# Kernel tuning notes

Measured on AMD Instinct MI355X. Metric: run time of the kernel, lower is better.

Reference implementation:

```python
import jax, jax.numpy as jnp
import numpy as np

B, S_SRC, T, D, H, DFF, NC, L = 8, 256, 64, 256, 8, 1024, 128, 2
HD = D // H
EPS = 1e-5


def _pe(length, d):
    pos = jnp.arange(length, dtype=jnp.float32)[:, None]
    div = jnp.exp(jnp.arange(0, d, 2, dtype=jnp.float32) * (-np.log(10000.0) / d))
    pe = jnp.zeros((length, d), dtype=jnp.float32)
    pe = pe.at[:, 0::2].set(jnp.sin(pos * div))
    pe = pe.at[:, 1::2].set(jnp.cos(pos * div))
    return pe


def setup_inputs() -> dict:
    key = jax.random.key(0)
    ks = jax.random.split(key, 16)
    s = 0.02
    rn = lambda k, shape: jax.random.normal(k, shape, dtype=jnp.float32) * s
    return {
        "encoder_output": jax.random.normal(ks[0], (B, S_SRC, D), dtype=jnp.float32),
        "emb_w": rn(ks[1], (D, NC)), "emb_b": jnp.zeros((D,), jnp.float32),
        "sa_wqkv": rn(ks[2], (L, 3 * D, D)), "sa_bqkv": jnp.zeros((L, 3 * D), jnp.float32),
        "sa_wo": rn(ks[3], (L, D, D)), "sa_bo": jnp.zeros((L, D), jnp.float32),
        "ca_wqkv": rn(ks[4], (L, 3 * D, D)), "ca_bqkv": jnp.zeros((L, 3 * D), jnp.float32),
        "ca_wo": rn(ks[5], (L, D, D)), "ca_bo": jnp.zeros((L, D), jnp.float32),
        "ln1_g": jnp.ones((L, D), jnp.float32), "ln1_b": jnp.zeros((L, D), jnp.float32),
        "ln2_g": jnp.ones((L, D), jnp.float32), "ln2_b": jnp.zeros((L, D), jnp.float32),
        "ffn_w1": rn(ks[6], (L, DFF, D)), "ffn_b1": jnp.zeros((L, DFF), jnp.float32),
        "ffn_w2": rn(ks[7], (L, D, DFF)), "ffn_b2": jnp.zeros((L, D), jnp.float32),
        "ln3_g": jnp.ones((L, D), jnp.float32), "ln3_b": jnp.zeros((L, D), jnp.float32),
        "op_w1": rn(ks[8], (D, D)), "op_b1": jnp.zeros((D,), jnp.float32),
        "bn_g": jnp.ones((D,), jnp.float32), "bn_b": jnp.zeros((D,), jnp.float32),
        "op_w2": rn(ks[9], (NC, D)), "op_b2": jnp.zeros((NC,), jnp.float32),
        "tgt_length": T,
    }


def _ln(x, g, b):
    m = x.mean(-1, keepdims=True)
    v = ((x - m) ** 2).mean(-1, keepdims=True)
    return (x - m) * jax.lax.rsqrt(v + EPS) * g + b


def _heads(x):  # [B,T,D] -> [B,H,T,HD]
    b, t, _ = x.shape
    return x.reshape(b, t, H, HD).transpose(0, 2, 1, 3)


def _merge(x):  # [B,H,T,HD] -> [B,T,D]
    return x.transpose(0, 2, 1, 3).reshape(x.shape[0], -1, D)


def _forward(encoder_output, emb_w, emb_b, sa_wqkv, sa_bqkv, sa_wo, sa_bo,
             ca_wqkv, ca_bqkv, ca_wo, ca_bo, ln1_g, ln1_b, ln2_g, ln2_b,
             ffn_w1, ffn_b1, ffn_w2, ffn_b2, ln3_g, ln3_b,
             op_w1, op_b1, bn_g, bn_b, op_w2, op_b2, tgt_length):
    Tq = tgt_length
    pe = _pe(Tq, D)
    scale = 1.0 / np.sqrt(HD)
    causal = jnp.where(jnp.arange(Tq)[:, None] >= jnp.arange(Tq)[None, :], 0.0, -1e9).astype(jnp.float32)
    # cross-attention K/V from encoder memory (constant across decode steps)
    mem_kv = jnp.einsum('bsd,led->lbse', encoder_output, ca_wqkv[:, D:, :]) + ca_bqkv[:, None, None, D:]
    mem_k = mem_kv[..., :D].reshape(L, B, S_SRC, H, HD).transpose(0, 1, 3, 2, 4)
    mem_v = mem_kv[..., D:].reshape(L, B, S_SRC, H, HD).transpose(0, 1, 3, 2, 4)

    def decode_full(buf):  # buf [B,Tq,NC] -> logits [B,Tq,NC]
        x = buf @ emb_w.T + emb_b + pe[None]
        for l in range(L):
            qkv = x @ sa_wqkv[l].T + sa_bqkv[l]
            q, k, v = (_heads(qkv[..., i * D:(i + 1) * D]) for i in range(3))
            att = jax.nn.softmax(jnp.einsum('bhqe,bhke->bhqk', q, k) * scale + causal, axis=-1)
            o = _merge(jnp.einsum('bhqk,bhke->bhqe', att, v)) @ sa_wo[l].T + sa_bo[l]
            x = _ln(x + o, ln1_g[l], ln1_b[l])
            qc = _heads(x @ ca_wqkv[l, :D].T + ca_bqkv[l, :D])
            attc = jax.nn.softmax(jnp.einsum('bhqe,bhke->bhqk', qc, mem_k[l]) * scale, axis=-1)
            oc = _merge(jnp.einsum('bhqk,bhke->bhqe', attc, mem_v[l])) @ ca_wo[l].T + ca_bo[l]
            x = _ln(x + oc, ln2_g[l], ln2_b[l])
            f = jax.nn.relu(x @ ffn_w1[l].T + ffn_b1[l]) @ ffn_w2[l].T + ffn_b2[l]
            x = _ln(x + f, ln3_g[l], ln3_b[l])
        y = x @ op_w1.T + op_b1
        # eval-mode BatchNorm1d with running stats (0, 1): pure affine
        y = jax.nn.relu(y * (1.0 / np.sqrt(1.0 + EPS)) * bn_g + bn_b)
        return y @ op_w2.T + op_b2

    def step(buf, t):
        out = decode_full(buf)                                   # [B,Tq,NC]
        y_t = jax.lax.dynamic_slice_in_dim(out, t, 1, axis=1)    # [B,1,NC]
        buf = jax.lax.dynamic_update_slice_in_dim(buf, y_t, jnp.minimum(t + 1, Tq - 1), axis=1)
        return buf, y_t[:, 0]

    buf0 = jnp.zeros((B, Tq, NC), dtype=jnp.float32)  # decoder_input starts as zeros
    _, ys = jax.lax.scan(step, buf0, jnp.arange(Tq))
    return ys.transpose(1, 0, 2)  # [B,Tq,NC]


def reference(encoder_output, emb_w, emb_b, sa_wqkv, sa_bqkv, sa_wo, sa_bo,
              ca_wqkv, ca_bqkv, ca_wo, ca_bo, ln1_g, ln1_b, ln2_g, ln2_b,
              ffn_w1, ffn_b1, ffn_w2, ffn_b2, ln3_g, ln3_b,
              op_w1, op_b1, bn_g, bn_b, op_w2, op_b2, tgt_length):
    return _forward(encoder_output, emb_w, emb_b, sa_wqkv, sa_bqkv, sa_wo, sa_bo,
                    ca_wqkv, ca_bqkv, ca_wo, ca_bo, ln1_g, ln1_b, ln2_g, ln2_b,
                    ffn_w1, ffn_b1, ffn_w2, ffn_b2, ln3_g, ln3_b,
                    op_w1, op_b1, bn_g, bn_b, op_w2, op_b2, tgt_length)
```

## Files before the change

### kernel.cpp

```cpp
#include <hip/hip_runtime.h>
#include <math.h>


#define EPS_ 1e-5f
#define SCALE_ 0.17677669529663687f
#define BNS 0.99999500003749969f
#define DEV __device__ __forceinline__
#define DYNF 36864

#define D4(a,b) ((a).x*(b).x+(a).y*(b).y+(a).z*(b).z+(a).w*(b).w)
#define F4(p)  (*(float4*)(p))
#define CF4(p) (*(const float4*)(p))

DEV float ald(const float* p){return __hip_atomic_load(p,__ATOMIC_RELAXED,__HIP_MEMORY_SCOPE_AGENT);}
DEV void  ast(float* p,float v){__hip_atomic_store(p,v,__ATOMIC_RELAXED,__HIP_MEMORY_SCOPE_AGENT);}
DEV int   aldi(const int* p){return __hip_atomic_load(p,__ATOMIC_RELAXED,__HIP_MEMORY_SCOPE_AGENT);}
DEV void  asti(int* p,int v){__hip_atomic_store(p,v,__ATOMIC_RELAXED,__HIP_MEMORY_SCOPE_AGENT);}

DEV float wsum(float v){
#pragma unroll
  for(int o=32;o;o>>=1) v+=__shfl_xor(v,o,64);
  return v;
}
DEV float wmax(float v){
#pragma unroll
  for(int o=32;o;o>>=1) v=fmaxf(v,__shfl_xor(v,o,64));
  return v;
}

DEV void waitflags(const int* base,int n,int s){
  if((int)threadIdx.x<64){
    const int* p=base+threadIdx.x*32;
    bool need=(int)threadIdx.x<n;
    int v=need?aldi(p):0x7fffffff;
    while(!__all(v>=s)){ v=need?aldi(p):0x7fffffff; }
  }
  __syncthreads();
}

template<int NB>
DEV void ln_reg(float (&v)[NB],const float* __restrict__ g,
                const float* __restrict__ bb,float* red){
  int tid=threadIdx.x,wid=tid>>6,lane=tid&63;
  float s[NB],s2[NB];
#pragma unroll
  for(int r=0;r<NB;++r){ s[r]=wsum(v[r]); s2[r]=wsum(v[r]*v[r]); }
  if(lane==0){
#pragma unroll
    for(int r=0;r<NB;++r){ red[r*4+wid]=s[r]; red[NB*4+r*4+wid]=s2[r]; }
  }
  __syncthreads();
  float gv=g[tid],bv=bb[tid];
#pragma unroll
  for(int r=0;r<NB;++r){
    float S=red[r*4+0]+red[r*4+1]+red[r*4+2]+red[r*4+3];
    float S2=red[NB*4+r*4+0]+red[NB*4+r*4+1]+red[NB*4+r*4+2]+red[NB*4+r*4+3];
    float m=S*(1.f/256.f);
    float rs=rsqrtf(S2*(1.f/256.f)-m*m+EPS_);
    v[r]=(v[r]-m)*rs*gv+bv;
  }
}

template<int NB,int L>
DEV void role_s1(float* LDS,int h,int bs,
    const float* __restrict__ sa_wqkv,const float* __restrict__ sa_bqkv,
    const float* __restrict__ sa_wo,
    const float* __restrict__ ln2_g,const float* __restrict__ ln2_b,
    const float* __restrict__ ln3_g,const float* __restrict__ ln3_b,
    const float* __restrict__ ffn_b2,const float* __restrict__ emb_b,
    int* F1,const int* F3,const int* FX0,const int* FER2,int* FER3,
    float* kc,float* vc,const float* r2red,float* r3red,
    const float* p3,float* p1,const float* xrow){
  const int tid=threadIdx.x;
  float* W   =LDS;
  float* WO  =LDS+24960;
  float* XS  =LDS+34176;
  float* QKV =LDS+35200;
  float* SC  =LDS+35584;
  float* PART=LDS+35840;
  float* RED =LDS+36096;

  for(int idx=tid;idx<96*64;idx+=256){
    int row=idx>>6,i4=idx&63,which=row>>5,j=row&31;
    F4(&W[row*260+4*i4])=CF4(sa_wqkv+(size_t)L*196608+((size_t)(which*256+h*32+j))*256+4*i4);
  }
  for(int idx=tid;idx<256*8;idx+=256){
    int c=idx>>3,i=idx&7;
    F4(&WO[c*36+4*i])=CF4(sa_wo+(size_t)L*65536+(size_t)c*256+h*32+4*i);
  }
  __syncthreads();

  float dv=expf((float)(tid&~1)*(-9.210340371976184f/256.f));

  for(int t=0;t<64;++t){
    if(L==0){
      float aarg=(float)t*dv;
      float peb=emb_b[tid]+((tid&1)?cosf(aarg):sinf(aarg));
      waitflags(FX0+bs*32,NB,t);
#pragma unroll
      for(int bi=0;bi<NB;++bi) XS[bi*256+tid]=ald(xrow+(bs+bi)*256+tid)+peb;
      __syncthreads();
    }else{
      waitflags(FER2+bs*32,NB,t+1);
      float r2v[NB];
#pragma unroll
      for(int bi=0;bi<NB;++bi) r2v[bi]=ald(r2red+(bs+bi)*256+tid);
      ln_reg<NB>(r2v,ln2_g,ln2_b,RED);
      waitflags(F3+bs*16*32,NB*16,t+1);
      float p3v[NB][16];
#pragma unroll
      for(int bi=0;bi<NB;++bi)
#pragma unroll
        for(int cg=0;cg<16;++cg) p3v[bi][cg]=ald(p3+(cg*8+bs+bi)*256+tid);
      float r3v[NB];
      float fb=ffn_b2[tid];
#pragma unroll
      for(int bi=0;bi<NB;++bi){
        float s=0.f;
#pragma unroll
        for(int cg=0;cg<16;++cg) s+=p3v[bi][cg];
        r3v[bi]=r2v[bi]+s+fb;
      }
      if(h==0){
#pragma unroll
        for(int bi=0;bi<NB;++bi) ast(r3red+(bs+bi)*256+tid,r3v[bi]);
        __syncthreads();
        if(tid<NB) asti(FER3+(bs+tid)*32,t+1);
      }
      ln_reg<NB>(r3v,ln3_g,ln3_b,RED+32);
#pragma unroll
      for(int bi=0;bi<NB;++bi) XS[bi*256+tid]=r3v[bi];
      __syncthreads();
    }
    if(tid<192){
      int row=tid>>1,kq=tid&1;
      float a[NB];
#pragma unroll
      for(int bi=0;bi<NB;++bi) a[bi]=0.f;
#pragma unroll
      for(int i=0;i<32;++i){
        float4 w=F4(&W[row*260+kq*128+4*i]);
#pragma unroll
        for(int bi=0;bi<NB;++bi) a[bi]+=D4(w,F4(&XS[bi*256+kq*128+4*i]));
      }
#pragma unroll
      for(int bi=0;bi<NB;++bi) a[bi]+=__shfl_down(a[bi],1,64);
      if(kq==0){
        int which=row>>5,j=row&31;
        float bias=sa_bqkv[L*768+which*256+h*32+j];
#pragma unroll
        for(int bi=0;bi<NB;++bi){
          float v=a[bi]+bias;
          if(which==0) QKV[bi*96+j]=v;
          else{
            int off=(which==1)?32:64;
            QKV[bi*96+off+j]=v;
            float* cache=(which==1)?kc:vc;
            cache[(((size_t)L*64+(bs+bi)*8+h)*64+t)*32+j]=v;
          }
        }
      }
    }
    __syncthreads();
    {
      int bi=(tid>>6)&(NB-1),key=tid&63;
      float s=-3.0e38f;
      if(key<=t){
        float a=0.f;
        if(key==t){
#pragma unroll
          for(int i=0;i<8;++i) a+=D4(F4(&QKV[bi*96+4*i]),F4(&QKV[bi*96+32+4*i]));
        }else{
          const float4* kr=(const float4*)(kc+(((size_t)L*64+(bs+bi)*8+h)*64+key)*32);
#pragma unroll
          for(int i=0;i<8;++i) a+=D4(F4(&QKV[bi*96+4*i]),kr[i]);
        }
        s=a*SCALE_;
      }
      float mx=wmax(s);
      float e=(key<=t)?expf(s-mx):0.f;
      float sm=wsum(e);
      SC[bi*64+key]=e/sm;
    }
    __syncthreads();
    {
      int bi=(tid>>6)&(NB-1),lane=tid&63,gg=lane>>5,col=lane&31;
      float acc=0.f;
      int k0=gg*32,k1=min(k0+32,t+1);
      for(int k=k0;k<k1;++k){
        float vv=(k==t)?QKV[bi*96+64+col]
                       :vc[(((size_t)L*64+(bs+bi)*8+h)*64+k)*32+col];
        acc+=SC[bi*64+k]*vv;
      }
      PART[bi*64+gg*32+col]=acc;
    }
    __syncthreads();
    if(tid<NB*32){
      int bi=tid>>5,col=tid&31;
      QKV[bi*96+col]=PART[bi*64+col]+PART[bi*64+32+col];
    }
    __syncthreads();
    {
      float a[NB];
#pragma unroll
      for(int bi=0;bi<NB;++bi) a[bi]=0.f;
#pragma unroll
      for(int i=0;i<8;++i){
        float4 w=F4(&WO[tid*36+4*i]);
#pragma unroll
        for(int bi=0;bi<NB;++bi) a[bi]+=D4(w,F4(&QKV[bi*96+4*i]));
      }
#pragma unroll
      for(int bi=0;bi<NB;++bi) ast(p1+(h*8+bs+bi)*256+tid,a[bi]);
    }
    __syncthreads();
    if(tid<NB) asti(F1+((L*8+bs+tid)*8+h)*32,t+1);
  }
}

DEV void role_s2(float* LDS,int rid,
    const float* __restrict__ enc,
    const float* __restrict__ ca_wqkv,const float* __restrict__ ca_bqkv,
    const float* __restrict__ ca_wo,
    const float* __restrict__ ln1_g,const float* __restrict__ ln1_b,
    const float* __restrict__ ln3_g,const float* __restrict__ ln3_b,
    const float* __restrict__ sa_bo,const float* __restrict__ emb_b,
    const int* F1,int* F2,const int* FX0,const int* FER3,int* FER1,
    const float* r3red,float* r1red,const float* p1,float* p2,const float* xrow){
  const int tid=threadIdx.x;
  const int b=rid>>4,h=(rid>>1)&7,l=rid&1;
  float* WQ  =LDS;
  float* WO  =LDS+8320;
  float* MK  =LDS+17536;
  float* MV  =LDS+26752;
  float* XS  =LDS+35968;
  float* PS  =LDS+36224;
  float* PART=LDS+36480;
  float* QC  =LDS+36736;
  float* RED =LDS+36784;

  for(int idx=tid;idx<64*64;idx+=256){
    int row=idx>>6,i4=idx&63;
    int grow=(row<32)?(256+h*32+row):(512+h*32+row-32);
    F4(&LDS[row*260+4*i4])=CF4(ca_wqkv+(size_t)l*196608+(size_t)grow*256+4*i4);
  }
  __syncthreads();
  for(int p=0;p<2;++p){
    int s=p*128+(tid>>1),kh=tid&1;
    float4 er[32];
#pragma unroll
    for(int i=0;i<32;++i) er[i]=CF4(enc+((size_t)(b*256+s))*256+kh*128+4*i);
    for(int out=0;out<64;++out){
      float a=0.f;
#pragma unroll
      for(int i=0;i<32;++i) a+=D4(F4(&LDS[out*260+kh*128+4*i]),er[i]);
      a+=__shfl_down(a,1,64);
      if(kh==0){
        if(out<32) MK[s*36+out]    =a+ca_bqkv[l*768+256+h*32+out];
        else       MV[s*36+out-32] =a+ca_bqkv[l*768+512+h*32+out-32];
      }
    }
  }
  __syncthreads();
  for(int idx=tid;idx<32*64;idx+=256){
    int row=idx>>6,i4=idx&63;
    F4(&WQ[row*260+4*i4])=CF4(ca_wqkv+(size_t)l*196608+(size_t)(h*32+row)*256+4*i4);
  }
  for(int idx=tid;idx<256*8;idx+=256){
    int c=idx>>3,i=idx&7;
    F4(&WO[c*36+4*i])=CF4(ca_wo+(size_t)l*65536+(size_t)c*256+h*32+4*i);
  }
  __syncthreads();

  float dv=expf((float)(tid&~1)*(-9.210340371976184f/256.f));

  for(int t=0;t<64;++t){
    float xv;
    if(l==0){
      float aarg=(float)t*dv;
      float peb=emb_b[tid]+((tid&1)?cosf(aarg):sinf(aarg));
      waitflags(FX0+b*32,1,t);
      xv=ald(xrow+b*256+tid)+peb;
    }else{
      waitflags(FER3+b*32,1,t+1);
      float t0[1]={ald(r3red+b*256+tid)};
      ln_reg<1>(t0,ln3_g,ln3_b,RED);
      xv=t0[0];
    }
    waitflags(F1+(l*8+b)*8*32,8,t+1);
    float p1v[8];
#pragma unroll
    for(int h2=0;h2<8;++h2) p1v[h2]=ald(p1+(h2*8+b)*256+tid);
    float r1v=xv+sa_bo[l*256+tid];
#pragma unroll
    for(int h2=0;h2<8;++h2) r1v+=p1v[h2];
    if(h==0){
      ast(r1red+l*2048+b*256+tid,r1v);
      __syncthreads();
      if(tid==0) asti(FER1+(l*8+b)*32,t+1);
    }
    float t1[1]={r1v};
    ln_reg<1>(t1,ln1_g+l*256,ln1_b+l*256,RED+8);
    XS[tid]=t1[0];
    __syncthreads();
    {
      int col=tid>>3,g=tid&7;
      float a=0.f;
#pragma unroll
      for(int i=0;i<8;++i) a+=D4(F4(&WQ[col*260+g*32+4*i]),F4(&XS[g*32+4*i]));
      a+=__shfl_down(a,4,64);a+=__shfl_down(a,2,64);a+=__shfl_down(a,1,64);
      if(g==0) QC[col]=a+ca_bqkv[l*768+h*32+col];
    }
    __syncthreads();
    {
      float a=0.f;
#pragma unroll
      for(int i=0;i<8;++i) a+=D4(F4(&MK[tid*36+4*i]),F4(&QC[4*i]));
      float sv=a*SCALE_;
      int wid=tid>>6,lane=tid&63;
      float mw=wmax(sv);
      float e=expf(sv-mw);
      float sw=wsum(e);
      if(lane==0){RED[16+wid]=mw;RED[20+wid]=sw;}
      __syncthreads();
      float M=fmaxf(fmaxf(RED[16],RED[17]),fmaxf(RED[18],RED[19]));
      float tot=RED[20]*expf(RED[16]-M)+RED[21]*expf(RED[17]-M)
               +RED[22]*expf(RED[18]-M)+RED[23]*expf(RED[19]-M);
      PS[tid]=e*expf(mw-M)/tot;
    }
    __syncthreads();
    {
      int gg=tid>>5,col=tid&31;
      float acc=0.f;
      for(int s2=gg*32;s2<gg*32+32;++s2) acc+=PS[s2]*MV[s2*36+col];
      PART[gg*32+col]=acc;
    }
    __syncthreads();
    if(tid<32){
      float o=0.f;
#pragma unroll
      for(int g2=0;g2<8;++g2) o+=PART[g2*32+tid];
      QC[tid]=o;
    }
    __syncthreads();
    {
      float a=0.f;
#pragma unroll
      for(int i=0;i<8;++i) a+=D4(F4(&WO[tid*36+4*i]),F4(&QC[4*i]));
      ast(p2+(h*8+b)*256+tid,a);
    }
    __syncthreads();
    if(tid==0) asti(F2+((l*8+b)*8+h)*32,t+1);
  }
}

DEV void role_s3(float* LDS,int rid,
    const float* __restrict__ ffn_w1,const float* __restrict__ ffn_b1,
    const float* __restrict__ ffn_w2,
    const float* __restrict__ ln1_g,const float* __restrict__ ln1_b,
    const float* __restrict__ ln2_g,const float* __restrict__ ln2_b,
    const float* __restrict__ ca_bo,
    const int* F2,int* F3,const int* FER1,int* FER2,
    const float* r1red,float* r2red,const float* p2,float* p3){
  const int tid=threadIdx.x;
  const int l=rid>>5,cg=(rid>>1)&15,bh=rid&1,bs=bh*4;
  float* W1 =LDS;
  float* W2T=LDS+16640;
  float* X4 =LDS+33280;
  float* HH =LDS+34304;
  float* RED=LDS+34576;

  for(int idx=tid;idx<64*64;idx+=256){
    int row=idx>>6,i4=idx&63;
    F4(&W1[row*260+4*i4])=CF4(ffn_w1+(size_t)l*262144+(size_t)(cg*64+row)*256+4*i4);
  }
  for(int idx=tid;idx<256*16;idx+=256){
    int cc=idx>>4,k4=idx&15;
    float4 w=CF4(ffn_w2+(size_t)l*262144+(size_t)cc*1024+cg*64+4*k4);
    W2T[(4*k4+0)*260+cc]=w.x;W2T[(4*k4+1)*260+cc]=w.y;
    W2T[(4*k4+2)*260+cc]=w.z;W2T[(4*k4+3)*260+cc]=w.w;
  }
  __syncthreads();

  for(int t=0;t<64;++t){
    waitflags(FER1+(l*8+bs)*32,4,t+1);
    float r1v[4];
#pragma unroll
    for(int bi=0;bi<4;++bi) r1v[bi]=ald(r1red+l*2048+(bs+bi)*256+tid);
    ln_reg<4>(r1v,ln1_g+l*256,ln1_b+l*256,RED);
    waitflags(F2+(l*8+bs)*8*32,32,t+1);
    float p2v[4][8];
#pragma unroll
    for(int bi=0;bi<4;++bi)
#pragma unroll
      for(int h2=0;h2<8;++h2) p2v[bi][h2]=ald(p2+(h2*8+bs+bi)*256+tid);
    float r2v[4];
    float cb=ca_bo[l*256+tid];
#pragma unroll
    for(int bi=0;bi<4;++bi){
      float s=0.f;
#pragma unroll
      for(int h2=0;h2<8;++h2) s+=p2v[bi][h2];
      r2v[bi]=r1v[bi]+s+cb;
    }
    if(cg==0){
#pragma unroll
      for(int bi=0;bi<4;++bi) ast(r2red+l*2048+(bs+bi)*256+tid,r2v[bi]);
      __syncthreads();
      if(tid<4) asti(FER2+(l*8+bs+tid)*32,t+1);
    }
    ln_reg<4>(r2v,ln2_g+l*256,ln2_b+l*256,RED+32);
#pragma unroll
    for(int bi=0;bi<4;++bi) X4[bi*256+tid]=r2v[bi];
    __syncthreads();
    {
      int row=tid>>2,kq=tid&3;
      float a0=0.f,a1=0.f,a2=0.f,a3=0.f;
#pragma unroll
      for(int i=0;i<16;++i){
        float4 w=F4(&W1[row*260+kq*64+4*i]);
        a0+=D4(w,F4(&X4[0*256+kq*64+4*i]));a1+=D4(w,F4(&X4[1*256+kq*64+4*i]));
        a2+=D4(w,F4(&X4[2*256+kq*64+4*i]));a3+=D4(w,F4(&X4[3*256+kq*64+4*i]));
      }
      a0+=__shfl_down(a0,2,64);a0+=__shfl_down(a0,1,64);
      a1+=__shfl_down(a1,2,64);a1+=__shfl_down(a1,1,64);
      a2+=__shfl_down(a2,2,64);a2+=__shfl_down(a2,1,64);
      a3+=__shfl_down(a3,2,64);a3+=__shfl_down(a3,1,64);
      if(kq==0){
        float b1v=ffn_b1[l*1024+cg*64+row];
        HH[0*68+row]=fmaxf(a0+b1v,0.f);HH[1*68+row]=fmaxf(a1+b1v,0.f);
        HH[2*68+row]=fmaxf(a2+b1v,0.f);HH[3*68+row]=fmaxf(a3+b1v,0.f);
      }
    }
    __syncthreads();
    {
      int chunk=tid&63,bi=tid>>6;
      float ax=0.f,ay=0.f,az=0.f,aw=0.f;
      for(int k=0;k<64;++k){
        float4 w=F4(&W2T[k*260+4*chunk]);
        float hv=HH[bi*68+k];
        ax+=w.x*hv;ay+=w.y*hv;az+=w.z*hv;aw+=w.w*hv;
      }
      float* dst=p3+(size_t)l*32768+(size_t)(cg*8+bs+bi)*256+4*chunk;
      ast(dst+0,ax);ast(dst+1,ay);ast(dst+2,az);ast(dst+3,aw);
    }
    __syncthreads();
    if(tid<4) asti(F3+((l*8+bs+tid)*16+cg)*32,t+1);
  }
}

DEV void role_head(float* LDS,int b,
    const float* __restrict__ op_w1,const float* __restrict__ op_b1,
    const float* __restrict__ bn_g,const float* __restrict__ bn_b,
    const float* __restrict__ op_w2,const float* __restrict__ op_b2,
    const float* __restrict__ emb_w,
    const float* __restrict__ ln2_g,const float* __restrict__ ln2_b,
    const float* __restrict__ ln3_g,const float* __restrict__ ln3_b,
    const float* __restrict__ ffn_b2,
    const int* F3,int* FX0,const int* FER2,
    const float* r2red,const float* p3,float* xrow,float* outp){
  const int tid=threadIdx.x;
  float* X  =LDS;
  float* Y  =LDS+256;
  float* LG =LDS+512;
  float* RED=LDS+768;

  for(int t=0;t<64;++t){
    waitflags(FER2+(8+b)*32,1,t+1);
    float t0[1]={ald(r2red+2048+b*256+tid)};
    ln_reg<1>(t0,ln2_g+256,ln2_b+256,RED);
    waitflags(F3+(8+b)*16*32,16,t+1);
    float p3v[16];
#pragma unroll
    for(int cg=0;cg<16;++cg) p3v[cg]=ald(p3+32768+(cg*8+b)*256+tid);
    float r3=t0[0]+ffn_b2[256+tid];
#pragma unroll
    for(int cg=0;cg<16;++cg) r3+=p3v[cg];
    float t1[1]={r3};
    ln_reg<1>(t1,ln3_g+256,ln3_b+256,RED+8);
    X[tid]=t1[0];
    __syncthreads();
    {
      int g=tid&15,cc=tid>>4;
      for(int it=0;it<16;++it){
        int c2=it*16+cc;
        const float4* w4=(const float4*)(op_w1+(size_t)c2*256+g*16);
        const float4* x4=(const float4*)(X+g*16);
        float a=0.f;
#pragma unroll
        for(int i=0;i<4;++i) a+=D4(w4[i],x4[i]);
        a+=__shfl_down(a,8,64);a+=__shfl_down(a,4,64);
        a+=__shfl_down(a,2,64);a+=__shfl_down(a,1,64);
        if(g==0){
          float y=a+op_b1[c2];
          Y[c2]=fmaxf(y*BNS*bn_g[c2]+bn_b[c2],0.f);
        }
      }
    }
    __syncthreads();
    {
      int g=tid&15,cc=tid>>4;
      for(int it=0;it<8;++it){
        int c2=it*16+cc;
        const float4* w4=(const float4*)(op_w2+(size_t)c2*256+g*16);
        const float4* y4=(const float4*)(Y+g*16);
        float a=0.f;
#pragma unroll
        for(int i=0;i<4;++i) a+=D4(w4[i],y4[i]);
        a+=__shfl_down(a,8,64);a+=__shfl_down(a,4,64);
        a+=__shfl_down(a,2,64);a+=__shfl_down(a,1,64);
        if(g==0){
          float v=a+op_b2[c2];
          LG[c2]=v;
          outp[((size_t)b*64+t)*128+c2]=v;
        }
      }
    }
    __syncthreads();
    if(t<63){
      int g=tid&7,cc=tid>>3;
      for(int it=0;it<8;++it){
        int c2=it*32+cc;
        const float4* w4=(const float4*)(emb_w+(size_t)c2*128+g*16);
        const float4* l4=(const float4*)(LG+g*16);
        float a=0.f;
#pragma unroll
        for(int i=0;i<4;++i) a+=D4(w4[i],l4[i]);
        a+=__shfl_down(a,4,64);a+=__shfl_down(a,2,64);a+=__shfl_down(a,1,64);
        if(g==0) ast(xrow+b*256+c2,a);
      }
    }
    __syncthreads();
    if(tid==0) asti(FX0+b*32,t+1);
  }
}


__global__ void __launch_bounds__(256,1) k_decode(
    const float* enc,const float* emb_w,const float* emb_b,
    const float* sa_wqkv,const float* sa_bqkv,const float* sa_wo,const float* sa_bo,
    const float* ca_wqkv,const float* ca_bqkv,const float* ca_wo,const float* ca_bo,
    const float* ln1_g,const float* ln1_b,const float* ln2_g,const float* ln2_b,
    const float* ffn_w1,const float* ffn_b1,const float* ffn_w2,const float* ffn_b2,
    const float* ln3_g,const float* ln3_b,
    const float* op_w1,const float* op_b1,const float* bn_g,const float* bn_b,
    const float* op_w2,const float* op_b2,
    int* FX0,int* FER1,int* FER2,int* FER3,int* F1,int* F2,int* F3,
    float* xrow,float* kc,float* vc,float* r1red,float* r2red,float* r3red,
    float* p1,float* p2,float* p3,float* outp){
  __shared__ __align__(16) float LDS[DYNF];
  const int blk=blockIdx.x;
  if(blk<16){
    role_s1<4,0>(LDS,blk>>1,(blk&1)*4,sa_wqkv,sa_bqkv,sa_wo,ln2_g,ln2_b,ln3_g,ln3_b,
                 ffn_b2,emb_b,F1,F3,FX0,FER2,FER3,kc,vc,r2red,r3red,p3,p1,xrow);
  }else if(blk<48){
    int r=blk-16;
    role_s1<2,1>(LDS,r>>2,(r&3)*2,sa_wqkv,sa_bqkv,sa_wo,ln2_g,ln2_b,ln3_g,ln3_b,
                 ffn_b2,emb_b,F1,F3,FX0,FER2,FER3,kc,vc,r2red,r3red,p3,p1,xrow);
  }else if(blk<176){
    role_s2(LDS,blk-48,enc,ca_wqkv,ca_bqkv,ca_wo,ln1_g,ln1_b,ln3_g,ln3_b,sa_bo,emb_b,
            F1,F2,FX0,FER3,FER1,r3red,r1red,p1,p2,xrow);
  }else if(blk<240){
    role_s3(LDS,blk-176,ffn_w1,ffn_b1,ffn_w2,ln1_g,ln1_b,ln2_g,ln2_b,ca_bo,
            F2,F3,FER1,FER2,r1red,r2red,p2,p3);
  }else{
    role_head(LDS,blk-240,op_w1,op_b1,bn_g,bn_b,op_w2,op_b2,emb_w,
              ln2_g,ln2_b,ln3_g,ln3_b,ffn_b2,F3,FX0,FER2,r2red,p3,xrow,outp);
  }
}


extern "C" void kernel_launch(void* const* d_in, const int* in_sizes, int n_in,
                              void* d_out, int out_size, void* d_ws, size_t ws_size,
                              hipStream_t stream) {
  (void)in_sizes;(void)n_in;(void)out_size;(void)ws_size;
  const float* enc     =(const float*)d_in[0];
  const float* emb_w   =(const float*)d_in[1];
  const float* emb_b   =(const float*)d_in[2];
  const float* sa_wqkv =(const float*)d_in[3];
  const float* sa_bqkv =(const float*)d_in[4];
  const float* sa_wo   =(const float*)d_in[5];
  const float* sa_bo   =(const float*)d_in[6];
  const float* ca_wqkv =(const float*)d_in[7];
  const float* ca_bqkv =(const float*)d_in[8];
  const float* ca_wo   =(const float*)d_in[9];
  const float* ca_bo   =(const float*)d_in[10];
  const float* ln1_g   =(const float*)d_in[11];
  const float* ln1_b   =(const float*)d_in[12];
  const float* ln2_g   =(const float*)d_in[13];
  const float* ln2_b   =(const float*)d_in[14];
  const float* ffn_w1  =(const float*)d_in[15];
  const float* ffn_b1  =(const float*)d_in[16];
  const float* ffn_w2  =(const float*)d_in[17];
  const float* ffn_b2  =(const float*)d_in[18];
  const float* ln3_g   =(const float*)d_in[19];
  const float* ln3_b   =(const float*)d_in[20];
  const float* op_w1   =(const float*)d_in[21];
  const float* op_b1   =(const float*)d_in[22];
  const float* bn_g    =(const float*)d_in[23];
  const float* bn_b    =(const float*)d_in[24];
  const float* op_w2   =(const float*)d_in[25];
  const float* op_b2   =(const float*)d_in[26];

  float* out=(float*)d_out;

  int* I=(int*)d_ws;
  int* FX0 =I;
  int* FER1=I+256;
  int* FER2=I+768;
  int* FER3=I+1280;
  int* F1  =I+1536;
  int* F2  =I+5632;
  int* F3  =I+9728;
  hipMemsetAsync(d_ws,0,17920*4+2048*4,stream);

  float* F=(float*)d_ws+17920;
  float* xrow =F;
  float* kc   =xrow+2048;
  float* vc   =kc+262144;
  float* r1red=vc+262144;
  float* r2red=r1red+4096;
  float* r3red=r2red+4096;
  float* p1   =r3red+2048;
  float* p2   =p1+16384;
  float* p3   =p2+16384;

  k_decode<<<248,256,0,stream>>>(
      enc,emb_w,emb_b,sa_wqkv,sa_bqkv,sa_wo,sa_bo,
      ca_wqkv,ca_bqkv,ca_wo,ca_bo,ln1_g,ln1_b,ln2_g,ln2_b,
      ffn_w1,ffn_b1,ffn_w2,ffn_b2,ln3_g,ln3_b,
      op_w1,op_b1,bn_g,bn_b,op_w2,op_b2,
      FX0,FER1,FER2,FER3,F1,F2,F3,
      xrow,kc,vc,r1red,r2red,r3red,p1,p2,p3,out);
}
```

Before: 3.607 ms.

## Replace flag-based inter-block sync with tagged 64-bit value+epoch words

```diff
diff --git a/kernel.cpp b/kernel.cpp
--- a/kernel.cpp
+++ b/kernel.cpp
@@ -8,14 +8,46 @@
 #define DEV __device__ __forceinline__
 #define DYNF 36864
 
+typedef unsigned long long u64;
+
 #define D4(a,b) ((a).x*(b).x+(a).y*(b).y+(a).z*(b).z+(a).w*(b).w)
 #define F4(p)  (*(float4*)(p))
 #define CF4(p) (*(const float4*)(p))
 
-DEV float ald(const float* p){return __hip_atomic_load(p,__ATOMIC_RELAXED,__HIP_MEMORY_SCOPE_AGENT);}
-DEV void  ast(float* p,float v){__hip_atomic_store(p,v,__ATOMIC_RELAXED,__HIP_MEMORY_SCOPE_AGENT);}
-DEV int   aldi(const int* p){return __hip_atomic_load(p,__ATOMIC_RELAXED,__HIP_MEMORY_SCOPE_AGENT);}
-DEV void  asti(int* p,int v){__hip_atomic_store(p,v,__ATOMIC_RELAXED,__HIP_MEMORY_SCOPE_AGENT);}
+DEV u64  ald64(const u64* p){return __hip_atomic_load(p,__ATOMIC_RELAXED,__HIP_MEMORY_SCOPE_AGENT);}
+DEV void ast64(u64* p,u64 v){__hip_atomic_store(p,v,__ATOMIC_RELAXED,__HIP_MEMORY_SCOPE_AGENT);}
+DEV u64   mkw(float v,int s){return ((u64)(unsigned)s<<32)|(u64)__float_as_uint(v);}
+DEV int   tg(u64 w){return (int)(unsigned)(w>>32);}
+DEV float vlw(u64 w){return __uint_as_float((unsigned)w);}
+
+DEV float poll1(const u64* p,int s){
+  u64 w=ald64(p);
+  while(tg(w)!=s) w=ald64(p);
+  return vlw(w);
+}
+template<int N>
+DEV void pollv(const u64* p0,int stride,int s,float* out){
+  while(true){
+    bool ok=true;
+#pragma unroll
+    for(int i=0;i<N;++i){u64 w=ald64(p0+(size_t)i*stride);ok&=(tg(w)==s);out[i]=vlw(w);}
+    if(ok) return;
+  }
+}
+template<int NB,int N>
+DEV void psum2(const u64* p0,int sb,int sn,int s,float* acc){
+  while(true){
+    bool ok=true;
+#pragma unroll
+    for(int b2=0;b2<NB;++b2){
+      float a=0.f;
+#pragma unroll
+      for(int i=0;i<N;++i){u64 w=ald64(p0+(size_t)b2*sb+(size_t)i*sn);ok&=(tg(w)==s);a+=vlw(w);}
+      acc[b2]=a;
+    }
+    if(ok) return;
+  }
+}
 
 DEV float wsum(float v){
 #pragma unroll
@@ -26,16 +58,6 @@
 #pragma unroll
   for(int o=32;o;o>>=1) v=fmaxf(v,__shfl_xor(v,o,64));
   return v;
-}
-
-DEV void waitflags(const int* base,int n,int s){
-  if((int)threadIdx.x<64){
-    const int* p=base+threadIdx.x*32;
-    bool need=(int)threadIdx.x<n;
-    int v=need?aldi(p):0x7fffffff;
-    while(!__all(v>=s)){ v=need?aldi(p):0x7fffffff; }
-  }
-  __syncthreads();
 }
 
 template<int NB>
@@ -68,9 +90,8 @@
     const float* __restrict__ ln2_g,const float* __restrict__ ln2_b,
     const float* __restrict__ ln3_g,const float* __restrict__ ln3_b,
     const float* __restrict__ ffn_b2,const float* __restrict__ emb_b,
-    int* F1,const int* F3,const int* FX0,const int* FER2,int* FER3,
-    float* kc,float* vc,const float* r2red,float* r3red,
-    const float* p3,float* p1,const float* xrow){
+    float* kc,float* vc,
+    const u64* r2T,u64* r3T,const u64* p3T,u64* p1T,const u64* xrowT){
   const int tid=threadIdx.x;
   float* W   =LDS;
   float* WO  =LDS+24960;
@@ -93,39 +114,28 @@
   float dv=expf((float)(tid&~1)*(-9.210340371976184f/256.f));
 
   for(int t=0;t<64;++t){
+    const int fv=2*t+L+1;
     if(L==0){
       float aarg=(float)t*dv;
       float peb=emb_b[tid]+((tid&1)?cosf(aarg):sinf(aarg));
-      waitflags(FX0+bs*32,NB,t);
-#pragma unroll
-      for(int bi=0;bi<NB;++bi) XS[bi*256+tid]=ald(xrow+(bs+bi)*256+tid)+peb;
+      float xv[NB];
+      pollv<NB>(xrowT+bs*256+tid,256,t,xv);
+#pragma unroll
+      for(int bi=0;bi<NB;++bi) XS[bi*256+tid]=xv[bi]+peb;
       __syncthreads();
     }else{
-      waitflags(FER2+bs*32,NB,t+1);
       float r2v[NB];
-#pragma unroll
-      for(int bi=0;bi<NB;++bi) r2v[bi]=ald(r2red+(bs+bi)*256+tid);
+      pollv<NB>(r2T+bs*256+tid,256,fv-1,r2v);
       ln_reg<NB>(r2v,ln2_g,ln2_b,RED);
-      waitflags(F3+bs*16*32,NB*16,t+1);
-      float p3v[NB][16];
-#pragma unroll
-      for(int bi=0;bi<NB;++bi)
-#pragma unroll
-        for(int cg=0;cg<16;++cg) p3v[bi][cg]=ald(p3+(cg*8+bs+bi)*256+tid);
+      float s3[NB];
+      psum2<NB,16>(p3T+bs*256+tid,256,2048,fv-1,s3);
       float r3v[NB];
       float fb=ffn_b2[tid];
 #pragma unroll
-      for(int bi=0;bi<NB;++bi){
-        float s=0.f;
-#pragma unroll
-        for(int cg=0;cg<16;++cg) s+=p3v[bi][cg];
-        r3v[bi]=r2v[bi]+s+fb;
-      }
+      for(int bi=0;bi<NB;++bi) r3v[bi]=r2v[bi]+s3[bi]+fb;
       if(h==0){
 #pragma unroll
-        for(int bi=0;bi<NB;++bi) ast(r3red+(bs+bi)*256+tid,r3v[bi]);
-        __syncthreads();
-        if(tid<NB) asti(FER3+(bs+tid)*32,t+1);
+        for(int bi=0;bi<NB;++bi) ast64(r3T+(bs+bi)*256+tid,mkw(r3v[bi],t+1));
       }
       ln_reg<NB>(r3v,ln3_g,ln3_b,RED+32);
 #pragma unroll
@@ -211,10 +221,9 @@
         for(int bi=0;bi<NB;++bi) a[bi]+=D4(w,F4(&QKV[bi*96+4*i]));
       }
 #pragma unroll
-      for(int bi=0;bi<NB;++bi) ast(p1+(h*8+bs+bi)*256+tid,a[bi]);
-    }
-    __syncthreads();
-    if(tid<NB) asti(F1+((L*8+bs+tid)*8+h)*32,t+1);
+      for(int bi=0;bi<NB;++bi) ast64(p1T+(h*8+bs+bi)*256+tid,mkw(a[bi],fv));
+    }
+    __syncthreads();
   }
 }
 
@@ -225,8 +234,7 @@
     const float* __restrict__ ln1_g,const float* __restrict__ ln1_b,
     const float* __restrict__ ln3_g,const float* __restrict__ ln3_b,
     const float* __restrict__ sa_bo,const float* __restrict__ emb_b,
-    const int* F1,int* F2,const int* FX0,const int* FER3,int* FER1,
-    const float* r3red,float* r1red,const float* p1,float* p2,const float* xrow){
+    const u64* p1T,u64* p2T,u64* r1T,const u64* r3T,const u64* xrowT){
   const int tid=threadIdx.x;
   const int b=rid>>4,h=(rid>>1)&7,l=rid&1;
   float* WQ  =LDS;
@@ -275,30 +283,21 @@
   float dv=expf((float)(tid&~1)*(-9.210340371976184f/256.f));
 
   for(int t=0;t<64;++t){
+    const int fv=2*t+l+1;
     float xv;
     if(l==0){
       float aarg=(float)t*dv;
       float peb=emb_b[tid]+((tid&1)?cosf(aarg):sinf(aarg));
-      waitflags(FX0+b*32,1,t);
-      xv=ald(xrow+b*256+tid)+peb;
+      xv=poll1(xrowT+b*256+tid,t)+peb;
     }else{
-      waitflags(FER3+b*32,1,t+1);
-      float t0[1]={ald(r3red+b*256+tid)};
+      float t0[1]={poll1(r3T+b*256+tid,t+1)};
       ln_reg<1>(t0,ln3_g,ln3_b,RED);
       xv=t0[0];
     }
-    waitflags(F1+(l*8+b)*8*32,8,t+1);
-    float p1v[8];
-#pragma unroll
-    for(int h2=0;h2<8;++h2) p1v[h2]=ald(p1+(h2*8+b)*256+tid);
-    float r1v=xv+sa_bo[l*256+tid];
-#pragma unroll
-    for(int h2=0;h2<8;++h2) r1v+=p1v[h2];
-    if(h==0){
-      ast(r1red+l*2048+b*256+tid,r1v);
-      __syncthreads();
-      if(tid==0) asti(FER1+(l*8+b)*32,t+1);
-    }
+    float s1[1];
+    psum2<1,8>(p1T+b*256+tid,0,2048,fv,s1);
+    float r1v=xv+s1[0]+sa_bo[l*256+tid];
+    if(h==0) ast64(r1T+l*2048+b*256+tid,mkw(r1v,fv));
     float t1[1]={r1v};
     ln_reg<1>(t1,ln1_g+l*256,ln1_b+l*256,RED+8);
     XS[tid]=t1[0];
@@ -347,10 +346,9 @@
       float a=0.f;
 #pragma unroll
       for(int i=0;i<8;++i) a+=D4(F4(&WO[tid*36+4*i]),F4(&QC[4*i]));
-      ast(p2+(h*8+b)*256+tid,a);
-    }
-    __syncthreads();
-    if(tid==0) asti(F2+((l*8+b)*8+h)*32,t+1);
+      ast64(p2T+(h*8+b)*256+tid,mkw(a,fv));
+    }
+    __syncthreads();
   }
 }
 
@@ -360,8 +358,7 @@
     const float* __restrict__ ln1_g,const float* __restrict__ ln1_b,
     const float* __restrict__ ln2_g,const float* __restrict__ ln2_b,
     const float* __restrict__ ca_bo,
-    const int* F2,int* F3,const int* FER1,int* FER2,
-    const float* r1red,float* r2red,const float* p2,float* p3){
+    const u64* p2T,u64* p3T,const u64* r1T,u64* r2T){
   const int tid=threadIdx.x;
   const int l=rid>>5,cg=(rid>>1)&15,bh=rid&1,bs=bh*4;
   float* W1 =LDS;
@@ -383,31 +380,19 @@
   __syncthreads();
 
   for(int t=0;t<64;++t){
-    waitflags(FER1+(l*8+bs)*32,4,t+1);
+    const int fv=2*t+l+1;
     float r1v[4];
-#pragma unroll
-    for(int bi=0;bi<4;++bi) r1v[bi]=ald(r1red+l*2048+(bs+bi)*256+tid);
+    pollv<4>(r1T+l*2048+bs*256+tid,256,fv,r1v);
     ln_reg<4>(r1v,ln1_g+l*256,ln1_b+l*256,RED);
-    waitflags(F2+(l*8+bs)*8*32,32,t+1);
-    float p2v[4][8];
-#pragma unroll
-    for(int bi=0;bi<4;++bi)
-#pragma unroll
-      for(int h2=0;h2<8;++h2) p2v[bi][h2]=ald(p2+(h2*8+bs+bi)*256+tid);
+    float s2v[4];
+    psum2<4,8>(p2T+bs*256+tid,256,2048,fv,s2v);
     float r2v[4];
     float cb=ca_bo[l*256+tid];
 #pragma unroll
-    for(int bi=0;bi<4;++bi){
-      float s=0.f;
-#pragma unroll
-      for(int h2=0;h2<8;++h2) s+=p2v[bi][h2];
-      r2v[bi]=r1v[bi]+s+cb;
-    }
+    for(int bi=0;bi<4;++bi) r2v[bi]=r1v[bi]+s2v[bi]+cb;
     if(cg==0){
 #pragma unroll
-      for(int bi=0;bi<4;++bi) ast(r2red+l*2048+(bs+bi)*256+tid,r2v[bi]);
-      __syncthreads();
-      if(tid<4) asti(FER2+(l*8+bs+tid)*32,t+1);
+      for(int bi=0;bi<4;++bi) ast64(r2T+l*2048+(bs+bi)*256+tid,mkw(r2v[bi],fv));
     }
     ln_reg<4>(r2v,ln2_g+l*256,ln2_b+l*256,RED+32);
 #pragma unroll
@@ -441,11 +426,11 @@
         float hv=HH[bi*68+k];
         ax+=w.x*hv;ay+=w.y*hv;az+=w.z*hv;aw+=w.w*hv;
       }
-      float* dst=p3+(size_t)l*32768+(size_t)(cg*8+bs+bi)*256+4*chunk;
-      ast(dst+0,ax);ast(dst+1,ay);ast(dst+2,az);ast(dst+3,aw);
-    }
-    __syncthreads();
-    if(tid<4) asti(F3+((l*8+bs+tid)*16+cg)*32,t+1);
+      u64* dst=p3T+(size_t)l*32768+(size_t)(cg*8+bs+bi)*256+4*chunk;
+      ast64(dst+0,mkw(ax,fv));ast64(dst+1,mkw(ay,fv));
+      ast64(dst+2,mkw(az,fv));ast64(dst+3,mkw(aw,fv));
+    }
+    __syncthreads();
   }
 }
 
@@ -457,8 +442,7 @@
     const float* __restrict__ ln2_g,const float* __restrict__ ln2_b,
     const float* __restrict__ ln3_g,const float* __restrict__ ln3_b,
     const float* __restrict__ ffn_b2,
-    const int* F3,int* FX0,const int* FER2,
-    const float* r2red,const float* p3,float* xrow,float* outp){
+    const u64* p3T,const u64* r2T,u64* xrowT,float* outp){
   const int tid=threadIdx.x;
   float* X  =LDS;
   float* Y  =LDS+256;
@@ -466,16 +450,12 @@
   float* RED=LDS+768;
 
   for(int t=0;t<64;++t){
-    waitflags(FER2+(8+b)*32,1,t+1);
-    float t0[1]={ald(r2red+2048+b*256+tid)};
+    const int fv=2*t+2;
+    float t0[1]={poll1(r2T+2048+b*256+tid,fv)};
     ln_reg<1>(t0,ln2_g+256,ln2_b+256,RED);
-    waitflags(F3+(8+b)*16*32,16,t+1);
-    float p3v[16];
-#pragma unroll
-    for(int cg=0;cg<16;++cg) p3v[cg]=ald(p3+32768+(cg*8+b)*256+tid);
-    float r3=t0[0]+ffn_b2[256+tid];
-#pragma unroll
-    for(int cg=0;cg<16;++cg) r3+=p3v[cg];
+    float s3[1];
+    psum2<1,16>(p3T+32768+b*256+tid,0,2048,fv,s3);
+    float r3=t0[0]+s3[0]+ffn_b2[256+tid];
     float t1[1]={r3};
     ln_reg<1>(t1,ln3_g+256,ln3_b+256,RED+8);
     X[tid]=t1[0];
@@ -527,11 +507,10 @@
 #pragma unroll
         for(int i=0;i<4;++i) a+=D4(w4[i],l4[i]);
         a+=__shfl_down(a,4,64);a+=__shfl_down(a,2,64);a+=__shfl_down(a,1,64);
-        if(g==0) ast(xrow+b*256+c2,a);
-      }
-    }
-    __syncthreads();
-    if(tid==0) asti(FX0+b*32,t+1);
+        if(g==0) ast64(xrowT+b*256+c2,mkw(a,t+1));
+      }
+    }
+    __syncthreads();
   }
 }
 
@@ -545,27 +524,26 @@
     const float* ln3_g,const float* ln3_b,
     const float* op_w1,const float* op_b1,const float* bn_g,const float* bn_b,
     const float* op_w2,const float* op_b2,
-    int* FX0,int* FER1,int* FER2,int* FER3,int* F1,int* F2,int* F3,
-    float* xrow,float* kc,float* vc,float* r1red,float* r2red,float* r3red,
-    float* p1,float* p2,float* p3,float* outp){
+    u64* xrowT,u64* r3T,u64* r1T,u64* r2T,u64* p1T,u64* p2T,u64* p3T,
+    float* kc,float* vc,float* outp){
   __shared__ __align__(16) float LDS[DYNF];
   const int blk=blockIdx.x;
   if(blk<16){
     role_s1<4,0>(LDS,blk>>1,(blk&1)*4,sa_wqkv,sa_bqkv,sa_wo,ln2_g,ln2_b,ln3_g,ln3_b,
-                 ffn_b2,emb_b,F1,F3,FX0,FER2,FER3,kc,vc,r2red,r3red,p3,p1,xrow);
+                 ffn_b2,emb_b,kc,vc,r2T,r3T,p3T,p1T,xrowT);
   }else if(blk<48){
     int r=blk-16;
     role_s1<2,1>(LDS,r>>2,(r&3)*2,sa_wqkv,sa_bqkv,sa_wo,ln2_g,ln2_b,ln3_g,ln3_b,
-                 ffn_b2,emb_b,F1,F3,FX0,FER2,FER3,kc,vc,r2red,r3red,p3,p1,xrow);
+                 ffn_b2,emb_b,kc,vc,r2T,r3T,p3T,p1T,xrowT);
   }else if(blk<176){
     role_s2(LDS,blk-48,enc,ca_wqkv,ca_bqkv,ca_wo,ln1_g,ln1_b,ln3_g,ln3_b,sa_bo,emb_b,
-            F1,F2,FX0,FER3,FER1,r3red,r1red,p1,p2,xrow);
+            p1T,p2T,r1T,r3T,xrowT);
   }else if(blk<240){
     role_s3(LDS,blk-176,ffn_w1,ffn_b1,ffn_w2,ln1_g,ln1_b,ln2_g,ln2_b,ca_bo,
-            F2,F3,FER1,FER2,r1red,r2red,p2,p3);
+            p2T,p3T,r1T,r2T);
   }else{
     role_head(LDS,blk-240,op_w1,op_b1,bn_g,bn_b,op_w2,op_b2,emb_w,
-              ln2_g,ln2_b,ln3_g,ln3_b,ffn_b2,F3,FX0,FER2,r2red,p3,xrow,outp);
+              ln2_g,ln2_b,ln3_g,ln3_b,ffn_b2,p3T,r2T,xrowT,outp);
   }
 }
 
@@ -604,32 +582,23 @@
 
   float* out=(float*)d_out;
 
-  int* I=(int*)d_ws;
-  int* FX0 =I;
-  int* FER1=I+256;
-  int* FER2=I+768;
-  int* FER3=I+1280;
-  int* F1  =I+1536;
-  int* F2  =I+5632;
-  int* F3  =I+9728;
-  hipMemsetAsync(d_ws,0,17920*4+2048*4,stream);
-
-  float* F=(float*)d_ws+17920;
-  float* xrow =F;
-  float* kc   =xrow+2048;
-  float* vc   =kc+262144;
-  float* r1red=vc+262144;
-  float* r2red=r1red+4096;
-  float* r3red=r2red+4096;
-  float* p1   =r3red+2048;
-  float* p2   =p1+16384;
-  float* p3   =p2+16384;
+  u64* T=(u64*)d_ws;
+  u64* xrowT=T;
+  u64* r3T  =T+2048;
+  u64* r1T  =T+4096;
+  u64* r2T  =T+8192;
+  u64* p1T  =T+12288;
+  u64* p2T  =T+28672;
+  u64* p3T  =T+45056;
+  hipMemsetAsync(d_ws,0,110592*sizeof(u64),stream);
+
+  float* kc=(float*)(T+110592);
+  float* vc=kc+262144;
 
   k_decode<<<248,256,0,stream>>>(
       enc,emb_w,emb_b,sa_wqkv,sa_bqkv,sa_wo,sa_bo,
       ca_wqkv,ca_bqkv,ca_wo,ca_bo,ln1_g,ln1_b,ln2_g,ln2_b,
       ffn_w1,ffn_b1,ffn_w2,ffn_b2,ln3_g,ln3_b,
       op_w1,op_b1,bn_g,bn_b,op_w2,op_b2,
-      FX0,FER1,FER2,FER3,F1,F2,F3,
-      xrow,kc,vc,r1red,r2red,r3red,p1,p2,p3,out);
-}
+      xrowT,r3T,r1T,r2T,p1T,p2T,p3T,kc,vc,out);
+}
```

Result: slower. 3.881 ms (+7.6%).
